# Performance work log

Hardware: AMD Instinct MI355X
Metric: run time of the kernel (lower is better)

The kernel has to match this reference:

```python
import jax, jax.numpy as jnp
import numpy as np

B, S, D, H = 2, 2048, 1024, 16
HD = D // H  # head dim = 64


def setup_inputs() -> dict:
    key = jax.random.key(0)
    ks = jax.random.split(key, 4)
    scale = 1.0 / np.sqrt(D)
    return {
        "hidden_states": jax.random.normal(ks[0], (B, S, D), dtype=jnp.float32),
        "attention_mask": jnp.zeros((B, 1, 1, S), dtype=jnp.float32),
        "Wq": jax.random.normal(ks[1], (D, D), dtype=jnp.float32) * scale,
        "bq": jnp.zeros((D,), dtype=jnp.float32),
        "Wk": jax.random.normal(ks[2], (D, D), dtype=jnp.float32) * scale,
        "bk": jnp.zeros((D,), dtype=jnp.float32),
        "Wv": jax.random.normal(ks[3], (D, D), dtype=jnp.float32) * scale,
        "bv": jnp.zeros((D,), dtype=jnp.float32),
    }


def reference(hidden_states, attention_mask, Wq, bq, Wk, bk, Wv, bv):
    b, s, d = hidden_states.shape
    # Q/K/V projections; torch nn.Linear computes x @ W.T + b
    def proj(W, bias):
        y = jnp.einsum('bsd,ed->bse', hidden_states, W) + bias
        return y.reshape(b, s, H, HD).transpose(0, 2, 1, 3)  # [b,h,s,hd]

    q = proj(Wq, bq)
    k = proj(Wk, bk)
    v = proj(Wv, bv)

    scores = jnp.einsum('bhqd,bhkd->bhqk', q, k) / jnp.sqrt(jnp.float32(HD))
    scores = scores + attention_mask  # additive mask broadcast [b,1,1,s]
    probs = jax.nn.softmax(scores, axis=-1)  # dropout p=0 (eval)
    ctx = jnp.einsum('bhqk,bhkd->bhqd', probs, v)
    ctx = ctx.transpose(0, 2, 1, 3).reshape(b, s, d)
    return ctx
```

## Files before the change

### kernel.cpp

```cpp
#include <hip/hip_runtime.h>
#include <hip/hip_bf16.h>

typedef __attribute__((ext_vector_type(4)))  float f32x4;
typedef __attribute__((ext_vector_type(16))) float f32x16;
typedef __bf16 bf16x8 __attribute__((ext_vector_type(8)));
typedef __attribute__((ext_vector_type(4))) unsigned int u32x4;
typedef __attribute__((ext_vector_type(4))) unsigned short u16x4;

#define MFMA16(a, b, c) __builtin_amdgcn_mfma_f32_16x16x32_bf16((a), (b), (c), 0, 0, 0)
#define MFMA32(a, b, c) __builtin_amdgcn_mfma_f32_32x32x16_bf16((a), (b), (c), 0, 0, 0)

#define LOG2E 1.4426950408889634f

#if __has_builtin(__builtin_amdgcn_exp2f)
#define EXP2(x) __builtin_amdgcn_exp2f(x)
#else
#define EXP2(x) exp2f(x)
#endif

static __device__ inline unsigned pk2(float a, float b) {
    unsigned short ua = __builtin_bit_cast(unsigned short, (__bf16)a);
    unsigned short ub = __builtin_bit_cast(unsigned short, (__bf16)b);
    return (unsigned)ua | ((unsigned)ub << 16);
}

static __device__ inline void plswap(unsigned& x, unsigned& y) {
#if __has_builtin(__builtin_amdgcn_permlane32_swap)
    auto r = __builtin_amdgcn_permlane32_swap((int)x, (int)y, false, false);
    x = (unsigned)r[0];
    y = (unsigned)r[1];
#else
    unsigned ox = (unsigned)__shfl_xor((int)x, 32);
    unsigned oy = (unsigned)__shfl_xor((int)y, 32);
    const bool lo = ((threadIdx.x & 63) < 32);
    unsigned nx = lo ? x : oy;
    unsigned ny = lo ? ox : y;
    x = nx; y = ny;
#endif
}

static __device__ inline void gll16(const void* g, void* l) {
    __builtin_amdgcn_global_load_lds(
        (const __attribute__((address_space(1))) void*)g,
        (__attribute__((address_space(3))) void*)l, 16, 0, 0);
}

__global__ __launch_bounds__(256) void to_bf16(
    const float* __restrict__ X,
    const float* __restrict__ Wq, const float* __restrict__ Wk,
    const float* __restrict__ Wv,
    __bf16* __restrict__ Xb, __bf16* __restrict__ Wb)
{
    const size_t i = ((size_t)blockIdx.x * 256 + threadIdx.x) * 8;
    const size_t MI = (size_t)1 << 20;
    const float* src;
    __bf16* dst;
    size_t off;
    if (i < 4 * MI)      { src = X;  dst = Xb;          off = i; }
    else if (i < 5 * MI) { src = Wq; dst = Wb;          off = i - 4 * MI; }
    else if (i < 6 * MI) { src = Wk; dst = Wb + MI;     off = i - 5 * MI; }
    else                 { src = Wv; dst = Wb + 2 * MI; off = i - 6 * MI; }

    f32x4 a = *reinterpret_cast<const f32x4*>(src + off);
    f32x4 b = *reinterpret_cast<const f32x4*>(src + off + 4);
    bf16x8 o;
    #pragma unroll
    for (int j = 0; j < 4; ++j) { o[j] = (__bf16)a[j]; o[4 + j] = (__bf16)b[j]; }
    *reinterpret_cast<bf16x8*>(dst + off) = o;
}

__global__ __launch_bounds__(256) void qkv_gemm(
    const __bf16* __restrict__ Xb, const __bf16* __restrict__ Wb,
    const float* __restrict__ bq, const float* __restrict__ bk,
    const float* __restrict__ bv,
    __bf16* __restrict__ Qb, __bf16* __restrict__ Kb, __bf16* __restrict__ Vt)
{
    const int z = blockIdx.z;
    const __bf16* W   = Wb + (size_t)z * (1u << 20);
    const float* bias = (z == 0) ? bq : (z == 1) ? bk : bv;
    const float oscale = (z == 0) ? (0.125f * LOG2E) : 1.0f;

    const int row0 = blockIdx.x * 128;
    const int col0 = blockIdx.y * 128;

    __shared__ __align__(16) char SMEM[34816];
    char* As = SMEM;
    char* Bs = SMEM + 16384;

    const int t    = threadIdx.x;
    const int lane = t & 63;
    const int w    = t >> 6;
    const int wr   = w >> 1, wc = w & 1;
    const int l15  = lane & 15, g = lane >> 4;

    f32x4 zero = {0.f, 0.f, 0.f, 0.f};
    f32x4 acc[4][4];
    #pragma unroll
    for (int m = 0; m < 4; ++m)
        #pragma unroll
        for (int n = 0; n < 4; ++n) acc[m][n] = zero;

    const int srow  = t >> 3;
    const int sinner = 16 * ((t & 7) ^ ((t >> 3) & 7));
    const char* srcA[4];
    const char* srcB[4];
    #pragma unroll
    for (int i = 0; i < 4; ++i) {
        srcA[i] = (const char*)Xb + (size_t)(row0 + i * 32 + srow) * 2048 + sinner;
        srcB[i] = (const char*)W  + (size_t)(col0 + i * 32 + srow) * 2048 + sinner;
    }
    const int ldst = t * 16;

    for (int k0 = 0; k0 < 2048; k0 += 128) {
        __syncthreads();
        #pragma unroll
        for (int i = 0; i < 4; ++i) {
            gll16(srcA[i] + k0, As + i * 4096 + ldst);
            gll16(srcB[i] + k0, Bs + i * 4096 + ldst);
        }
        __syncthreads();

        #pragma unroll
        for (int ksub = 0; ksub < 2; ++ksub) {
            const int cb2 = ksub * 64 + g * 16;
            bf16x8 af[4], bw[4];
            #pragma unroll
            for (int m = 0; m < 4; ++m) {
                const int row = wr * 64 + m * 16 + l15;
                af[m] = *reinterpret_cast<const bf16x8*>(
                    As + row * 128 + (cb2 ^ ((row & 7) << 4)));
            }
            #pragma unroll
            for (int n = 0; n < 4; ++n) {
                const int row = wc * 64 + n * 16 + l15;
                bw[n] = *reinterpret_cast<const bf16x8*>(
                    Bs + row * 128 + (cb2 ^ ((row & 7) << 4)));
            }
            #pragma unroll
            for (int m = 0; m < 4; ++m)
                #pragma unroll
                for (int n = 0; n < 4; ++n)
                    acc[m][n] = MFMA16(af[m], bw[n], acc[m][n]);
        }
    }

    if (z == 2) {
        __syncthreads();
        #pragma unroll
        for (int n = 0; n < 4; ++n) {
            const int e = wc * 64 + n * 16 + l15;
            const float bv_ = bias[col0 + e];
            #pragma unroll
            for (int m = 0; m < 4; ++m) {
                const int tok = wr * 64 + m * 16 + g * 4;
                u16x4 pk;
                #pragma unroll
                for (int j = 0; j < 4; ++j)
                    pk[j] = __builtin_bit_cast(unsigned short,
                                               (__bf16)(acc[m][n][j] + bv_));
                *reinterpret_cast<u16x4*>(SMEM + e * 272 + tok * 2) = pk;
            }
        }
        __syncthreads();
        const int r = t >> 1, seg = t & 1;
        const int e = col0 + r;
        const int h = e >> 6, hd = e & 63;
        const int bb = row0 >> 11;
        const int s0 = (row0 & 2047) + seg * 64;
        __bf16* dst = Vt + (((size_t)((bb * 16 + h) * 64 + hd)) << 11) + s0;
        const char* srcT = SMEM + r * 272 + seg * 128;
        #pragma unroll
        for (int i = 0; i < 8; ++i)
            *reinterpret_cast<bf16x8*>(dst + i * 8) =
                *reinterpret_cast<const bf16x8*>(srcT + i * 16);
    } else {
        __bf16* Ob = (z == 0) ? Qb : Kb;
        #pragma unroll
        for (int n = 0; n < 4; ++n) {
            const int e  = col0 + wc * 64 + n * 16 + l15;
            const float bv_ = bias[e];
            const int h = e >> 6, hd = e & 63;
            #pragma unroll
            for (int m = 0; m < 4; ++m) {
                #pragma unroll
                for (int j = 0; j < 4; ++j) {
                    const int tok = row0 + wr * 64 + m * 16 + g * 4 + j;
                    const int b = tok >> 11, s = tok & 2047;
                    const int bh = b * 16 + h;
                    Ob[((size_t)(bh * 2048 + s) << 6) | hd] =
                        (__bf16)((acc[m][n][j] + bv_) * oscale);
                }
            }
        }
    }
}

__global__ __launch_bounds__(256, 2) void flash_attn(
    const __bf16* __restrict__ Qb, const __bf16* __restrict__ Kb,
    const __bf16* __restrict__ Vt, const float* __restrict__ mask,
    float* __restrict__ out)
{
    const int bid = blockIdx.x;
    const int wid = (bid & 7) * 64 + (bid >> 3);
    const int qt  = wid & 15;
    const int bh  = wid >> 4;
    const int b = bh >> 4, h = bh & 15;

    const int t = threadIdx.x;
    const int lane = t & 63;
    const int w = t >> 6;
    const int l31 = lane & 31, hi = lane >> 5;
    const int q = (qt * 4 + w) * 32 + l31;

    __shared__ __align__(16) char KV[2][16384];
    __shared__ __align__(16) float mLs[2048];

    {
        const float* mb = mask + b * 2048 + t * 8;
        f32x4 m0 = *reinterpret_cast<const f32x4*>(mb);
        f32x4 m1 = *reinterpret_cast<const f32x4*>(mb + 4);
        *reinterpret_cast<f32x4*>(&mLs[t * 8])     = m0 * LOG2E;
        *reinterpret_cast<f32x4*>(&mLs[t * 8 + 4]) = m1 * LOG2E;
    }

    bf16x8 qf[4];
    {
        const __bf16* qp = Qb + ((size_t)(bh * 2048 + q) << 6) + hi * 8;
        #pragma unroll
        for (int ds = 0; ds < 4; ++ds)
            qf[ds] = *reinterpret_cast<const bf16x8*>(qp + ds * 16);
    }

    f32x16 ctx0, ctx1;
    #pragma unroll
    for (int r = 0; r < 16; ++r) { ctx0[r] = 0.f; ctx1[r] = 0.f; }
    float lrow = 0.f;

    const char* Kbase = (const char*)(Kb + ((size_t)bh << 17));
    const char* Vbase = (const char*)(Vt + ((size_t)bh << 17));
    const int xa = w * 1024 + lane * 16;
    const int xb = 4096 + w * 1024 + lane * 16;
    const char* srcKa = Kbase + (xa ^ (((xa >> 7) & 7) << 4));
    const char* srcKb = Kbase + (xb ^ (((xb >> 7) & 7) << 4));
    const char* srcVa = Vbase + (size_t)(xa >> 7) * 4096
                        + ((xa & 127) ^ (((xa >> 7) & 7) << 4));
    const char* srcVb = Vbase + (size_t)(xb >> 7) * 4096
                        + ((xb & 127) ^ (((xb >> 7) & 7) << 4));

    auto stage = [&](int buf, int kt) {
        char* L = &KV[buf][0];
        const size_t ko = (size_t)kt * 8192;
        const size_t vo = (size_t)kt * 128;
        gll16(srcKa + ko, L + w * 1024);
        gll16(srcKb + ko, L + 4096 + w * 1024);
        gll16(srcVa + vo, L + 8192 + w * 1024);
        gll16(srcVb + vo, L + 12288 + w * 1024);
    };

    const int swz = (l31 & 7) << 4;
    const int cb  = hi * 16;

    auto compute = [&](int buf, int kbase) {
        const char* KB = &KV[buf][0];
        bf16x8 kc[8];
        #pragma unroll
        for (int ds = 0; ds < 4; ++ds) {
            const int c = (ds * 32 + cb) ^ swz;
            kc[ds]     = *reinterpret_cast<const bf16x8*>(KB + l31 * 128 + c);
            kc[4 + ds] = *reinterpret_cast<const bf16x8*>(KB + (32 + l31) * 128 + c);
        }

        f32x16 pt0, pt1;
        #pragma unroll
        for (int c = 0; c < 4; ++c) {
            f32x4 mv0 = *reinterpret_cast<const f32x4*>(&mLs[kbase + 4 * hi + 8 * c]);
            f32x4 mv1 = *reinterpret_cast<const f32x4*>(&mLs[kbase + 32 + 4 * hi + 8 * c]);
            #pragma unroll
            for (int j = 0; j < 4; ++j) { pt0[4 * c + j] = mv0[j]; pt1[4 * c + j] = mv1[j]; }
        }

        __builtin_amdgcn_s_setprio(1);
        #pragma unroll
        for (int ds = 0; ds < 4; ++ds) {
            pt0 = MFMA32(kc[ds],     qf[ds], pt0);
            pt1 = MFMA32(kc[4 + ds], qf[ds], pt1);
        }
        __builtin_amdgcn_s_setprio(0);

        float ps = 0.f;
        #pragma unroll
        for (int r = 0; r < 16; ++r) {
            float e = EXP2(pt0[r]);
            pt0[r] = e; ps += e;
        }
        #pragma unroll
        for (int r = 0; r < 16; ++r) {
            float e = EXP2(pt1[r]);
            pt1[r] = e; ps += e;
        }
        ps += __shfl_xor(ps, 32);
        lrow += ps;

        const char* VB = KB + 8192;
        bf16x8 vv[8];
        #pragma unroll
        for (int ks = 0; ks < 4; ++ks) {
            const int c = (ks * 32 + cb) ^ swz;
            vv[ks]     = *reinterpret_cast<const bf16x8*>(VB + l31 * 128 + c);
            vv[4 + ks] = *reinterpret_cast<const bf16x8*>(VB + (32 + l31) * 128 + c);
        }

        __builtin_amdgcn_s_setprio(1);
        #pragma unroll
        for (int ks = 0; ks < 4; ++ks) {
            const f32x16& P = (ks < 2) ? pt0 : pt1;
            const int base = 8 * (ks & 1);
            unsigned a0 = pk2(P[base + 0], P[base + 1]);
            unsigned b0 = pk2(P[base + 4], P[base + 5]);
            unsigned a1 = pk2(P[base + 2], P[base + 3]);
            unsigned b1 = pk2(P[base + 6], P[base + 7]);
            plswap(a0, b0);
            plswap(a1, b1);
            u32x4 wv = {a0, a1, b0, b1};
            bf16x8 pb = __builtin_bit_cast(bf16x8, wv);
            ctx0 = MFMA32(vv[ks],     pb, ctx0);
            ctx1 = MFMA32(vv[4 + ks], pb, ctx1);
        }
        __builtin_amdgcn_s_setprio(0);
    };

    stage(0, 0);
    __syncthreads();
    for (int kt = 0; kt < 32; kt += 2) {
        stage(1, kt + 1);
        compute(0, kt * 64);
        __syncthreads();
        if (kt + 2 < 32) stage(0, kt + 2);
        compute(1, (kt + 1) * 64);
        __syncthreads();
    }

    const float inv = 1.0f / lrow;
    float* op = out + (((size_t)(b * 2048 + q)) << 10) + h * 64;
    #pragma unroll
    for (int c = 0; c < 4; ++c) {
        f32x4 s0v = {ctx0[4 * c + 0] * inv, ctx0[4 * c + 1] * inv,
                     ctx0[4 * c + 2] * inv, ctx0[4 * c + 3] * inv};
        f32x4 s1v = {ctx1[4 * c + 0] * inv, ctx1[4 * c + 1] * inv,
                     ctx1[4 * c + 2] * inv, ctx1[4 * c + 3] * inv};
        *reinterpret_cast<f32x4*>(op + 8 * c + 4 * hi)      = s0v;
        *reinterpret_cast<f32x4*>(op + 32 + 8 * c + 4 * hi) = s1v;
    }
}

extern "C" void kernel_launch(void* const* d_in, const int* in_sizes, int n_in,
                              void* d_out, int out_size, void* d_ws, size_t ws_size,
                              hipStream_t stream)
{
    const float* X    = (const float*)d_in[0];
    const float* mask = (const float*)d_in[1];
    const float* Wq   = (const float*)d_in[2];
    const float* bq   = (const float*)d_in[3];
    const float* Wk   = (const float*)d_in[4];
    const float* bk   = (const float*)d_in[5];
    const float* Wv   = (const float*)d_in[6];
    const float* bv   = (const float*)d_in[7];
    float* out = (float*)d_out;

    const size_t MI = (size_t)1 << 20;
    __bf16* Qb = (__bf16*)d_ws;
    __bf16* Kb = Qb + 4 * MI;
    __bf16* Vt = Kb + 4 * MI;
    __bf16* Xb = Vt + 4 * MI;
    __bf16* Wb = Xb + 4 * MI;

    to_bf16<<<dim3(3584), 256, 0, stream>>>(X, Wq, Wk, Wv, Xb, Wb);
    qkv_gemm<<<dim3(32, 8, 3), 256, 0, stream>>>(Xb, Wb, bq, bk, bv, Qb, Kb, Vt);
    flash_attn<<<dim3(512), 256, 0, stream>>>(Qb, Kb, Vt, mask, out);
}
```

Measured before the change: 97.32 us.

## Give each wave a private K tile and read V from global

```diff
diff --git a/kernel.cpp b/kernel.cpp
--- a/kernel.cpp
+++ b/kernel.cpp
@@ -212,7 +212,7 @@
     const int l31 = lane & 31, hi = lane >> 5;
     const int q = (qt * 4 + w) * 32 + l31;
 
-    __shared__ __align__(16) char KV[2][16384];
+    __shared__ __align__(16) char Ks[2][4][8192];
     __shared__ __align__(16) float mLs[2048];
 
     {
@@ -237,31 +237,40 @@
     float lrow = 0.f;
 
     const char* Kbase = (const char*)(Kb + ((size_t)bh << 17));
-    const char* Vbase = (const char*)(Vt + ((size_t)bh << 17));
-    const int xa = w * 1024 + lane * 16;
-    const int xb = 4096 + w * 1024 + lane * 16;
-    const char* srcKa = Kbase + (xa ^ (((xa >> 7) & 7) << 4));
-    const char* srcKb = Kbase + (xb ^ (((xb >> 7) & 7) << 4));
-    const char* srcVa = Vbase + (size_t)(xa >> 7) * 4096
-                        + ((xa & 127) ^ (((xa >> 7) & 7) << 4));
-    const char* srcVb = Vbase + (size_t)(xb >> 7) * 4096
-                        + ((xb & 127) ^ (((xb >> 7) & 7) << 4));
+    const __bf16* Vbh = Vt + ((size_t)bh << 17);
+    const char* srcK[8];
+    int xslot[8];
+    #pragma unroll
+    for (int i = 0; i < 8; ++i) {
+        const int x = i * 1024 + lane * 16;
+        xslot[i] = x;
+        srcK[i] = Kbase + (x ^ (((x >> 7) & 7) << 4));
+    }
 
     auto stage = [&](int buf, int kt) {
-        char* L = &KV[buf][0];
+        char* L = &Ks[buf][w][0];
         const size_t ko = (size_t)kt * 8192;
-        const size_t vo = (size_t)kt * 128;
-        gll16(srcKa + ko, L + w * 1024);
-        gll16(srcKb + ko, L + 4096 + w * 1024);
-        gll16(srcVa + vo, L + 8192 + w * 1024);
-        gll16(srcVb + vo, L + 12288 + w * 1024);
+        #pragma unroll
+        for (int i = 0; i < 8; ++i)
+            gll16(srcK[i] + ko, L + xslot[i]);
     };
 
     const int swz = (l31 & 7) << 4;
     const int cb  = hi * 16;
 
-    auto compute = [&](int buf, int kbase) {
-        const char* KB = &KV[buf][0];
+    auto compute = [&](int buf, int kt) {
+        const char* KB = &Ks[buf][w][0];
+        const int kbase = kt * 64;
+
+        const __bf16* vp0 = Vbh + ((size_t)l31 << 11) + kbase;
+        const __bf16* vp1 = Vbh + ((size_t)(32 + l31) << 11) + kbase;
+        bf16x8 vv[8];
+        #pragma unroll
+        for (int ks = 0; ks < 4; ++ks) {
+            vv[ks]     = *reinterpret_cast<const bf16x8*>(vp0 + ks * 16 + hi * 8);
+            vv[4 + ks] = *reinterpret_cast<const bf16x8*>(vp1 + ks * 16 + hi * 8);
+        }
+
         bf16x8 kc[8];
         #pragma unroll
         for (int ds = 0; ds < 4; ++ds) {
@@ -300,15 +309,6 @@
         }
         ps += __shfl_xor(ps, 32);
         lrow += ps;
-
-        const char* VB = KB + 8192;
-        bf16x8 vv[8];
-        #pragma unroll
-        for (int ks = 0; ks < 4; ++ks) {
-            const int c = (ks * 32 + cb) ^ swz;
-            vv[ks]     = *reinterpret_cast<const bf16x8*>(VB + l31 * 128 + c);
-            vv[4 + ks] = *reinterpret_cast<const bf16x8*>(VB + (32 + l31) * 128 + c);
-        }
 
         __builtin_amdgcn_s_setprio(1);
         #pragma unroll
@@ -331,13 +331,13 @@
 
     stage(0, 0);
     __syncthreads();
-    for (int kt = 0; kt < 32; kt += 2) {
-        stage(1, kt + 1);
-        compute(0, kt * 64);
-        __syncthreads();
-        if (kt + 2 < 32) stage(0, kt + 2);
-        compute(1, (kt + 1) * 64);
-        __syncthreads();
+
+    for (int kt = 0; kt < 32; ++kt) {
+        const int nk = (kt + 1 < 32) ? kt + 1 : 31;
+        stage((kt + 1) & 1, nk);
+        asm volatile("s_waitcnt vmcnt(8)" ::: "memory");
+        __builtin_amdgcn_sched_barrier(0);
+        compute(kt & 1, kt);
     }
 
     const float inv = 1.0f / lrow;
```

Measured after the change: 128.1 us. 1.32x slower.
